# Performance work log

Hardware: AMD Instinct MI355X
Metric: run time of the kernel (lower is better)

Reference implementation:

```python
import jax, jax.numpy as jnp
import numpy as np

D_DEC = 256  # decoder_size; W columns are [decoder | encoder] per the torch concat order


def setup_inputs() -> dict:
    key = jax.random.key(0)
    k1, k2, k3, k4 = jax.random.split(key, 4)
    B, S, E, D, A = 32, 4096, 256, 256, 256
    decoder_hidden = jax.random.normal(k1, (1, B, D), dtype=jnp.float32)
    encoder_outputs = jax.random.normal(k2, (S, B, E), dtype=jnp.float32)
    W = jax.random.normal(k3, (A, D + E), dtype=jnp.float32) / np.sqrt(D + E)
    b = jax.random.normal(k4, (A,), dtype=jnp.float32) * 0.02
    return {"decoder_hidden": decoder_hidden, "encoder_outputs": encoder_outputs, "W": W, "b": b}


def reference(decoder_hidden, encoder_outputs, W, b):
    # decoder_hidden: [1,B,D] -> [B,D]; encoder_outputs: [S,B,E] -> [B,S,E]
    dh = decoder_hidden[0]
    eo = jnp.transpose(encoder_outputs, (1, 0, 2))
    # Split the concat-linear: cat([dec, enc]) @ W.T == dec @ Wd.T + enc @ We.T
    Wd, We = W[:, :D_DEC], W[:, D_DEC:]
    # scores: tanh(linear) summed over attn dim -> [B,S]
    proj = dh @ Wd.T + b  # [B,A]
    attn = jnp.tanh(proj[:, None, :] + jnp.einsum('bse,ae->bsa', eo, We))
    scores = jnp.sum(attn, axis=2)  # [B,S]
    attn_softmax = jax.nn.softmax(scores, axis=1)  # [B,S]
    attended = jnp.einsum('bs,bse->be', attn_softmax, eo)  # [B,E]
    encoder_norms = jnp.linalg.norm(eo, axis=2)  # [B,S]
    attn_map = attn_softmax * encoder_norms
    return attended, attn_map
```

## Files before the change

kernel.cpp:

```cpp
#include <hip/hip_runtime.h>
#include <math.h>

#define B_  32
#define S_  4096
#define E_  256
#define A_  256
#define DE_ 512

typedef __attribute__((ext_vector_type(8))) short short8;
typedef __attribute__((ext_vector_type(4))) float f32x4;

__device__ inline unsigned short f2bf(float x) {
    unsigned int u = __float_as_uint(x);
    u += 0x7FFFu + ((u >> 16) & 1u);
    return (unsigned short)(u >> 16);
}
__device__ inline float tanh_fast(float x) {
    x = fminf(fmaxf(x, -15.f), 15.f);
    float t = __expf(2.f * x);
    return (t - 1.f) * __builtin_amdgcn_rcpf(t + 1.f);
}

__global__ __launch_bounds__(256) void prep_kernel(
    const float* __restrict__ W, const float* __restrict__ dh,
    const float* __restrict__ bias, unsigned short* __restrict__ wepk,
    float* __restrict__ proj, float* __restrict__ out)
{
    __shared__ float dh_lds[E_];
    const int bk  = blockIdx.x;
    const int tid = threadIdx.x;
    if (bk < 64) {
        const int idx = bk * 256 + tid;
        const int c     = idx >> 11;
        const int r     = idx & 2047;
        const int plane = r >> 10;
        const int kg    = (r >> 8) & 3;
        const int a     = r & 255;
        const float* src = W + (size_t)a * DE_ + E_ + c * 32 + kg * 8;
        unsigned int pk[4];
        #pragma unroll
        for (int j = 0; j < 4; ++j) {
            float x0 = src[2 * j], x1 = src[2 * j + 1];
            unsigned int u0 = __float_as_uint(x0) & 0xFFFF0000u;
            unsigned int u1 = __float_as_uint(x1) & 0xFFFF0000u;
            if (plane) {
                unsigned short l0 = f2bf(x0 - __uint_as_float(u0));
                unsigned short l1 = f2bf(x1 - __uint_as_float(u1));
                pk[j] = (unsigned int)l0 | ((unsigned int)l1 << 16);
            } else {
                pk[j] = (u0 >> 16) | u1;
            }
        }
        *(uint4*)&wepk[(size_t)idx * 8] = make_uint4(pk[0], pk[1], pk[2], pk[3]);
    } else if (bk < 96) {
        const int b = bk - 64;
        const int a = tid;
        dh_lds[a] = dh[b * E_ + a];
        __syncthreads();
        float acc = bias[a];
        const float* wrow = W + (size_t)a * DE_;
        #pragma unroll
        for (int d = 0; d < E_; d += 4) {
            float4 w = *(const float4*)(wrow + d);
            acc += dh_lds[d] * w.x + dh_lds[d+1] * w.y
                 + dh_lds[d+2] * w.z + dh_lds[d+3] * w.w;
        }
        proj[b * A_ + a] = acc;
    } else {
        #pragma unroll
        for (int j = tid; j < B_ * E_; j += 256) out[j] = 0.f;
    }
}

__global__ __launch_bounds__(256, 2) void scores_kernel(
    const float* __restrict__ eo, const unsigned short* __restrict__ wepk,
    const float* __restrict__ proj,
    float* __restrict__ scores, float* __restrict__ nsq)
{
    __shared__ __align__(16) unsigned char pool[49408];
    unsigned short* we_hl = (unsigned short*)pool;
    unsigned short* eo_hl = (unsigned short*)(pool + 32768);

    const int tid = threadIdx.x;
    const int b   = blockIdx.x & (B_ - 1);
    const int s0  = (blockIdx.x >> 5) * 128;
    const int w   = tid >> 6, l = tid & 63;
    const int lq  = l >> 4,  lr = l & 15;

    const int erow = tid >> 2;
    const int ekg  = tid & 3;
    const float* ebase = eo + (size_t)(s0 + erow) * (B_ * E_) + b * E_ + ekg * 8;

    f32x4 acc[8][4];
    #pragma unroll
    for (int i = 0; i < 8; ++i)
        #pragma unroll
        for (int j = 0; j < 4; ++j)
            acc[i][j] = (f32x4){0.f, 0.f, 0.f, 0.f};
    float nacc[2] = {0.f, 0.f};

    float4 ea0 = *(const float4*)(ebase);
    float4 ea1 = *(const float4*)(ebase + 4);
    float4 eb0 = *(const float4*)(ebase + (size_t)64 * (B_ * E_));
    float4 eb1 = *(const float4*)(ebase + (size_t)64 * (B_ * E_) + 4);

    for (int c = 0; c < 8; ++c) {
        __syncthreads();
        #pragma unroll
        for (int it = 0; it < 2; ++it) {
            float4 v0 = it ? eb0 : ea0;
            float4 v1 = it ? eb1 : ea1;
            nacc[it] += v0.x*v0.x + v0.y*v0.y + v0.z*v0.z + v0.w*v0.w
                      + v1.x*v1.x + v1.y*v1.y + v1.z*v1.z + v1.w*v1.w;
            float xs[8] = {v0.x, v0.y, v0.z, v0.w, v1.x, v1.y, v1.z, v1.w};
            unsigned int hp[4], lp[4];
            #pragma unroll
            for (int j = 0; j < 4; ++j) {
                unsigned int u0 = __float_as_uint(xs[2*j])   & 0xFFFF0000u;
                unsigned int u1 = __float_as_uint(xs[2*j+1]) & 0xFFFF0000u;
                hp[j] = (u0 >> 16) | u1;
                lp[j] = (unsigned int)f2bf(xs[2*j]   - __uint_as_float(u0))
                      | ((unsigned int)f2bf(xs[2*j+1] - __uint_as_float(u1)) << 16);
            }
            const int u = ekg * 130 + it * 64 + erow;
            *(uint4*)&eo_hl[(size_t)u * 8]         = make_uint4(hp[0], hp[1], hp[2], hp[3]);
            *(uint4*)&eo_hl[(size_t)(520 + u) * 8] = make_uint4(lp[0], lp[1], lp[2], lp[3]);
        }
        const unsigned short* gsrc = wepk + (size_t)c * 2048 * 8;
        #pragma unroll
        for (int it = 0; it < 8; ++it) {
            const int u = it * 256 + tid;
            __builtin_amdgcn_global_load_lds(
                (const __attribute__((address_space(1))) void*)(gsrc + (size_t)u * 8),
                (__attribute__((address_space(3))) void*)&we_hl[(size_t)u * 8],
                16, 0, 0);
        }
        __syncthreads();
        if (c < 7) {
            ea0 = *(const float4*)(ebase + (c + 1) * 32);
            ea1 = *(const float4*)(ebase + (c + 1) * 32 + 4);
            eb0 = *(const float4*)(ebase + (size_t)64 * (B_ * E_) + (c + 1) * 32);
            eb1 = *(const float4*)(ebase + (size_t)64 * (B_ * E_) + (c + 1) * 32 + 4);
        }
        short8 bh[4], bl[4];
        #pragma unroll
        for (int nt = 0; nt < 4; ++nt) {
            const int bunit = lq * 256 + w * 64 + nt * 16 + lr;
            bh[nt] = *(const short8*)&we_hl[(size_t)bunit * 8];
            bl[nt] = *(const short8*)&we_hl[(size_t)(1024 + bunit) * 8];
        }
        #pragma unroll
        for (int mt = 0; mt < 8; ++mt) {
            const int au = lq * 130 + mt * 16 + lr;
            short8 ah = *(const short8*)&eo_hl[(size_t)au * 8];
            short8 al = *(const short8*)&eo_hl[(size_t)(520 + au) * 8];
            #pragma unroll
            for (int nt = 0; nt < 4; ++nt) {
                acc[mt][nt] = __builtin_amdgcn_mfma_f32_16x16x32_bf16(ah, bh[nt], acc[mt][nt], 0, 0, 0);
                acc[mt][nt] = __builtin_amdgcn_mfma_f32_16x16x32_bf16(ah, bl[nt], acc[mt][nt], 0, 0, 0);
                acc[mt][nt] = __builtin_amdgcn_mfma_f32_16x16x32_bf16(al, bh[nt], acc[mt][nt], 0, 0, 0);
            }
        }
    }
    __syncthreads();

    float* red4  = (float*)pool;
    float* npart = (float*)(pool + 33280);
    float* qpart = (float*)(pool + 35328);
    float pr[4];
    #pragma unroll
    for (int nt = 0; nt < 4; ++nt) pr[nt] = proj[b * A_ + w * 64 + nt * 16 + lr];
    #pragma unroll
    for (int mt = 0; mt < 8; ++mt) {
        #pragma unroll
        for (int r = 0; r < 4; ++r) {
            float s = 0.f;
            #pragma unroll
            for (int nt = 0; nt < 4; ++nt)
                s += tanh_fast(pr[nt] + acc[mt][nt][r]);
            red4[(w * 16 + lr) * 130 + (mt * 16 + lq * 4 + r)] = s;
        }
    }
    npart[tid]       = nacc[0];
    npart[256 + tid] = nacc[1];
    __syncthreads();
    {
        const int row = tid >> 1, half = tid & 1;
        float s = 0.f;
        #pragma unroll
        for (int j = 0; j < 32; ++j) s += red4[(half * 32 + j) * 130 + row];
        qpart[half * 128 + row] = s;
    }
    __syncthreads();
    if (tid < 128) {
        scores[b * S_ + s0 + tid] = qpart[tid] + qpart[128 + tid];
        const int base = (tid < 64) ? 4 * tid : 256 + 4 * (tid - 64);
        nsq[b * S_ + s0 + tid] = npart[base] + npart[base + 1]
                               + npart[base + 2] + npart[base + 3];
    }
}

__global__ __launch_bounds__(256) void attend_kernel(
    const float* __restrict__ eo, const float* __restrict__ scores,
    const float* __restrict__ nsq, float* __restrict__ out)
{
    __shared__ float red[256];
    __shared__ float4 acc_red[4][64];
    const int tid = threadIdx.x;
    const int b   = blockIdx.x & (B_ - 1);
    const int ch  = blockIdx.x / B_;

    float v[16];
    float m = -1e30f;
    #pragma unroll
    for (int i = 0; i < 16; ++i) {
        v[i] = scores[b * S_ + i * 256 + tid];
        m = fmaxf(m, v[i]);
    }
    red[tid] = m;
    __syncthreads();
    for (int off = 128; off > 0; off >>= 1) {
        if (tid < off) red[tid] = fmaxf(red[tid], red[tid + off]);
        __syncthreads();
    }
    m = red[0];
    __syncthreads();
    float sum = 0.f;
    #pragma unroll
    for (int i = 0; i < 16; ++i) sum += __expf(v[i] - m);
    red[tid] = sum;
    __syncthreads();
    for (int off = 128; off > 0; off >>= 1) {
        if (tid < off) red[tid] += red[tid + off];
        __syncthreads();
    }
    const float inv = 1.f / red[0];

    const int le = tid & 63, sg = tid >> 6;
    const int s0 = ch * 128 + sg * 32;
    float4 a = make_float4(0.f, 0.f, 0.f, 0.f);
    #pragma unroll 8
    for (int s = 0; s < 32; ++s) {
        float pv = __expf(scores[b * S_ + s0 + s] - m) * inv;
        float4 e = *(const float4*)(eo + (size_t)(s0 + s) * (B_ * E_)
                                       + b * E_ + le * 4);
        a.x = fmaf(pv, e.x, a.x);
        a.y = fmaf(pv, e.y, a.y);
        a.z = fmaf(pv, e.z, a.z);
        a.w = fmaf(pv, e.w, a.w);
    }
    acc_red[sg][le] = a;
    if (tid < 128) {
        const int s = ch * 128 + tid;
        float pv = __expf(scores[b * S_ + s] - m) * inv;
        out[B_ * E_ + b * S_ + s] = pv * sqrtf(nsq[b * S_ + s]);
    }
    __syncthreads();
    if (tid < 64) {
        float4 a0 = acc_red[0][tid], a1 = acc_red[1][tid];
        float4 a2 = acc_red[2][tid], a3 = acc_red[3][tid];
        float* dst = out + b * E_ + tid * 4;
        atomicAdd(dst + 0, a0.x + a1.x + a2.x + a3.x);
        atomicAdd(dst + 1, a0.y + a1.y + a2.y + a3.y);
        atomicAdd(dst + 2, a0.z + a1.z + a2.z + a3.z);
        atomicAdd(dst + 3, a0.w + a1.w + a2.w + a3.w);
    }
}

extern "C" void kernel_launch(void* const* d_in, const int* in_sizes, int n_in,
                              void* d_out, int out_size, void* d_ws, size_t ws_size,
                              hipStream_t stream)
{
    const float* dh   = (const float*)d_in[0];
    const float* eo   = (const float*)d_in[1];
    const float* W    = (const float*)d_in[2];
    const float* bias = (const float*)d_in[3];
    float* out = (float*)d_out;
    float* ws  = (float*)d_ws;

    float* projb  = ws;
    float* nsqb   = ws + 8192;
    float* scores = nsqb + S_ * B_;
    unsigned short* wepk = (unsigned short*)(scores + S_ * B_);

    prep_kernel   <<<97,              256, 0, stream>>>(W, dh, bias, wepk, projb, out);
    scores_kernel <<<B_ * (S_ / 128), 256, 0, stream>>>(eo, wepk, projb, scores, nsqb);
    attend_kernel <<<B_ * (S_ / 128), 256, 0, stream>>>(eo, scores, nsqb, out);
}
```

Measured before the change: 258.5 us.

## Load W fragments directly to registers and split softmax stats into separate kernel

```diff
diff --git a/kernel.cpp b/kernel.cpp
--- a/kernel.cpp
+++ b/kernel.cpp
@@ -77,9 +77,8 @@
     const float* __restrict__ proj,
     float* __restrict__ scores, float* __restrict__ nsq)
 {
-    __shared__ __align__(16) unsigned char pool[49408];
-    unsigned short* we_hl = (unsigned short*)pool;
-    unsigned short* eo_hl = (unsigned short*)(pool + 32768);
+    __shared__ __align__(16) unsigned char pool[36352];
+    unsigned short* eo_hl = (unsigned short*)pool;
 
     const int tid = threadIdx.x;
     const int b   = blockIdx.x & (B_ - 1);
@@ -91,6 +90,8 @@
     const int ekg  = tid & 3;
     const float* ebase = eo + (size_t)(s0 + erow) * (B_ * E_) + b * E_ + ekg * 8;
 
+    const int wunit = lq * 256 + w * 64 + lr;
+
     f32x4 acc[8][4];
     #pragma unroll
     for (int i = 0; i < 8; ++i)
@@ -106,6 +107,15 @@
 
     for (int c = 0; c < 8; ++c) {
         __syncthreads();
+        short8 bh[4], bl[4];
+        {
+            const unsigned short* wsrc = wepk + (size_t)(c * 2048 + wunit) * 8;
+            #pragma unroll
+            for (int nt = 0; nt < 4; ++nt) {
+                bh[nt] = *(const short8*)(wsrc + (size_t)(nt * 16) * 8);
+                bl[nt] = *(const short8*)(wsrc + (size_t)(1024 + nt * 16) * 8);
+            }
+        }
         #pragma unroll
         for (int it = 0; it < 2; ++it) {
             float4 v0 = it ? eb0 : ea0;
@@ -126,15 +136,6 @@
             *(uint4*)&eo_hl[(size_t)u * 8]         = make_uint4(hp[0], hp[1], hp[2], hp[3]);
             *(uint4*)&eo_hl[(size_t)(520 + u) * 8] = make_uint4(lp[0], lp[1], lp[2], lp[3]);
         }
-        const unsigned short* gsrc = wepk + (size_t)c * 2048 * 8;
-        #pragma unroll
-        for (int it = 0; it < 8; ++it) {
-            const int u = it * 256 + tid;
-            __builtin_amdgcn_global_load_lds(
-                (const __attribute__((address_space(1))) void*)(gsrc + (size_t)u * 8),
-                (__attribute__((address_space(3))) void*)&we_hl[(size_t)u * 8],
-                16, 0, 0);
-        }
         __syncthreads();
         if (c < 7) {
             ea0 = *(const float4*)(ebase + (c + 1) * 32);
@@ -142,13 +143,6 @@
             eb0 = *(const float4*)(ebase + (size_t)64 * (B_ * E_) + (c + 1) * 32);
             eb1 = *(const float4*)(ebase + (size_t)64 * (B_ * E_) + (c + 1) * 32 + 4);
         }
-        short8 bh[4], bl[4];
-        #pragma unroll
-        for (int nt = 0; nt < 4; ++nt) {
-            const int bunit = lq * 256 + w * 64 + nt * 16 + lr;
-            bh[nt] = *(const short8*)&we_hl[(size_t)bunit * 8];
-            bl[nt] = *(const short8*)&we_hl[(size_t)(1024 + bunit) * 8];
-        }
         #pragma unroll
         for (int mt = 0; mt < 8; ++mt) {
             const int au = lq * 130 + mt * 16 + lr;
@@ -200,61 +194,71 @@
     }
 }
 
+__global__ __launch_bounds__(256) void stats_kernel(
+    const float* __restrict__ scores, float* __restrict__ nsq_pv,
+    float* __restrict__ out)
+{
+    __shared__ float red[256];
+    const int tid  = threadIdx.x;
+    const int b    = blockIdx.x & (B_ - 1);
+    const int part = blockIdx.x >> 5;
+    float v[16];
+    float m = -1e30f;
+    #pragma unroll
+    for (int i = 0; i < 16; ++i) {
+        v[i] = scores[b * S_ + i * 256 + tid];
+        m = fmaxf(m, v[i]);
+    }
+    red[tid] = m;
+    __syncthreads();
+    for (int off = 128; off > 0; off >>= 1) {
+        if (tid < off) red[tid] = fmaxf(red[tid], red[tid + off]);
+        __syncthreads();
+    }
+    m = red[0];
+    __syncthreads();
+    float sum = 0.f;
+    #pragma unroll
+    for (int i = 0; i < 16; ++i) sum += __expf(v[i] - m);
+    red[tid] = sum;
+    __syncthreads();
+    for (int off = 128; off > 0; off >>= 1) {
+        if (tid < off) red[tid] += red[tid + off];
+        __syncthreads();
+    }
+    const float inv = 1.f / red[0];
+    #pragma unroll
+    for (int j = 0; j < 2; ++j) {
+        const int i = part * 2 + j;
+        const int s = i * 256 + tid;
+        const float pv = __expf(v[i] - m) * inv;
+        out[B_ * E_ + b * S_ + s] = pv * sqrtf(nsq_pv[b * S_ + s]);
+        nsq_pv[b * S_ + s] = pv;
+    }
+}
+
 __global__ __launch_bounds__(256) void attend_kernel(
-    const float* __restrict__ eo, const float* __restrict__ scores,
-    const float* __restrict__ nsq, float* __restrict__ out)
-{
-    __shared__ float red[256];
+    const float* __restrict__ eo, const float* __restrict__ pv,
+    float* __restrict__ out)
+{
     __shared__ float4 acc_red[4][64];
     const int tid = threadIdx.x;
     const int b   = blockIdx.x & (B_ - 1);
     const int ch  = blockIdx.x / B_;
-
-    float v[16];
-    float m = -1e30f;
-    #pragma unroll
-    for (int i = 0; i < 16; ++i) {
-        v[i] = scores[b * S_ + i * 256 + tid];
-        m = fmaxf(m, v[i]);
-    }
-    red[tid] = m;
-    __syncthreads();
-    for (int off = 128; off > 0; off >>= 1) {
-        if (tid < off) red[tid] = fmaxf(red[tid], red[tid + off]);
-        __syncthreads();
-    }
-    m = red[0];
-    __syncthreads();
-    float sum = 0.f;
-    #pragma unroll
-    for (int i = 0; i < 16; ++i) sum += __expf(v[i] - m);
-    red[tid] = sum;
-    __syncthreads();
-    for (int off = 128; off > 0; off >>= 1) {
-        if (tid < off) red[tid] += red[tid + off];
-        __syncthreads();
-    }
-    const float inv = 1.f / red[0];
-
     const int le = tid & 63, sg = tid >> 6;
     const int s0 = ch * 128 + sg * 32;
     float4 a = make_float4(0.f, 0.f, 0.f, 0.f);
     #pragma unroll 8
     for (int s = 0; s < 32; ++s) {
-        float pv = __expf(scores[b * S_ + s0 + s] - m) * inv;
+        float p = pv[b * S_ + s0 + s];
         float4 e = *(const float4*)(eo + (size_t)(s0 + s) * (B_ * E_)
                                        + b * E_ + le * 4);
-        a.x = fmaf(pv, e.x, a.x);
-        a.y = fmaf(pv, e.y, a.y);
-        a.z = fmaf(pv, e.z, a.z);
-        a.w = fmaf(pv, e.w, a.w);
+        a.x = fmaf(p, e.x, a.x);
+        a.y = fmaf(p, e.y, a.y);
+        a.z = fmaf(p, e.z, a.z);
+        a.w = fmaf(p, e.w, a.w);
     }
     acc_red[sg][le] = a;
-    if (tid < 128) {
-        const int s = ch * 128 + tid;
-        float pv = __expf(scores[b * S_ + s] - m) * inv;
-        out[B_ * E_ + b * S_ + s] = pv * sqrtf(nsq[b * S_ + s]);
-    }
     __syncthreads();
     if (tid < 64) {
         float4 a0 = acc_red[0][tid], a1 = acc_red[1][tid];
@@ -285,5 +289,6 @@
 
     prep_kernel   <<<97,              256, 0, stream>>>(W, dh, bias, wepk, projb, out);
     scores_kernel <<<B_ * (S_ / 128), 256, 0, stream>>>(eo, wepk, projb, scores, nsqb);
-    attend_kernel <<<B_ * (S_ / 128), 256, 0, stream>>>(eo, scores, nsqb, out);
-}
+    stats_kernel  <<<B_ * 8,          256, 0, stream>>>(scores, nsqb, out);
+    attend_kernel <<<B_ * (S_ / 128), 256, 0, stream>>>(eo, nsqb, out);
+}
```

Result: no change. 261.4 us (+1.1%).
